# Optimization experiments

Measured on AMD Instinct MI355X. Metric: run time of the kernel, lower is better.

Reference implementation:

```python
import jax, jax.numpy as jnp
import numpy as np

L, D, H, F, K = 2, 256, 8, 512, 9
M, G1, G2, NT = 4, 40, 40, 2048
DH = D // H
KPD = 3  # per-dim neighbour window; KPD**2 == K


def setup_inputs() -> dict:
    key = jax.random.key(0)
    ks = jax.random.split(key, 16)
    s = 0.02
    ax0 = jnp.linspace(-1.0, 1.0, G1)
    ax1 = jnp.linspace(-1.0, 1.0, G2)
    gx, gy = jnp.meshgrid(ax0, ax1, indexing='ij')
    xc = jnp.broadcast_to(jnp.stack([gx, gy], -1), (M, G1, G2, 2))  # regular grid coords
    zc = jax.random.normal(ks[0], (M, G1, G2, D), dtype=jnp.float32)
    xt = jax.random.uniform(ks[1], (M, NT, 2), minval=-1.0, maxval=1.0)
    zt = jax.random.normal(ks[2], (M, NT, D), dtype=jnp.float32)
    def n(k, shape):
        return jax.random.normal(k, shape, dtype=jnp.float32) * s
    def ln():
        return jnp.stack([jnp.ones((L, D)), jnp.zeros((L, D))], 1)  # [L, 2(gamma,beta), D]
    return dict(
        xc=xc, zc=zc, xt=xt, zt=zt,
        sa_wqkv=n(ks[3], (L, D, 3 * D)), sa_wo=n(ks[4], (L, D, D)),
        sa_ln1=ln(), sa_ln2=ln(),
        sa_w1=n(ks[5], (L, D, F)), sa_b1=jnp.zeros((L, F)),
        sa_w2=n(ks[6], (L, F, D)), sa_b2=jnp.zeros((L, D)),
        ca_wq=n(ks[7], (L, D, D)), ca_wkv=n(ks[8], (L, D, 2 * D)), ca_wo=n(ks[9], (L, D, D)),
        ca_lnq=ln(), ca_lnkv=ln(), ca_ln2=ln(),
        ca_w1=n(ks[10], (L, D, F)), ca_b1=jnp.zeros((L, F)),
        ca_w2=n(ks[11], (L, F, D)), ca_b2=jnp.zeros((L, D)),
    )


def _ln(x, p):
    mu = x.mean(-1, keepdims=True)
    var = ((x - mu) ** 2).mean(-1, keepdims=True)
    return (x - mu) * jax.lax.rsqrt(var + 1e-5) * p[0] + p[1]


def nearest_gridded_neighbours(xt, xc):
    """Separable per-dim nearest grid index + KPD x KPD window, clamped at borders.
    Returns flat neighbour indices [M, NT, K] and validity mask [M, NT, K]."""
    ax0 = xc[:, :, 0, 0]  # [M, G1] axis-0 coordinates
    ax1 = xc[:, 0, :, 1]  # [M, G2] axis-1 coordinates
    n0 = jnp.argmin(jnp.abs(xt[..., 0:1] - ax0[:, None, :]), -1)  # [M, NT]
    n1 = jnp.argmin(jnp.abs(xt[..., 1:2] - ax1[:, None, :]), -1)
    off = jnp.arange(KPD) - KPD // 2
    r0 = n0[..., None] + off  # [M, NT, KPD]
    r1 = n1[..., None] + off
    v0 = (r0 >= 0) & (r0 < G1)
    v1 = (r1 >= 0) & (r1 < G2)
    i0 = jnp.clip(r0, 0, G1 - 1)
    i1 = jnp.clip(r1, 0, G2 - 1)
    idx = (i0[:, :, :, None] * G2 + i1[:, :, None, :]).reshape(xt.shape[0], -1, K)
    mask = (v0[:, :, :, None] & v1[:, :, None, :]).reshape(xt.shape[0], -1, K)
    return idx, mask


def reference(xc, zc, xt, zt, sa_wqkv, sa_wo, sa_ln1, sa_ln2, sa_w1, sa_b1, sa_w2, sa_b2,
              ca_wq, ca_wkv, ca_wo, ca_lnq, ca_lnkv, ca_ln2, ca_w1, ca_b1, ca_w2, ca_b2):
    m = zc.shape[0]
    idx, mask = nearest_gridded_neighbours(xt, xc)
    zc = zc.reshape(m, G1 * G2, D)  # flatten_grid
    bidx = jnp.arange(m)[:, None, None]
    scale = 1.0 / np.sqrt(DH)
    for l in range(L):
        # --- MHSA over flattened grid (pre-norm transformer block) ---
        h = _ln(zc, sa_ln1[l])
        q, k, v = jnp.split(h @ sa_wqkv[l], 3, -1)
        q = q.reshape(m, -1, H, DH); k = k.reshape(m, -1, H, DH); v = v.reshape(m, -1, H, DH)
        att = jax.nn.softmax(jnp.einsum('bnhd,bkhd->bhnk', q, k) * scale, -1)
        o = jnp.einsum('bhnk,bkhd->bnhd', att, v).reshape(m, -1, D)
        zc = zc + o @ sa_wo[l]
        h = _ln(zc, sa_ln2[l])
        zc = zc + jax.nn.gelu(h @ sa_w1[l] + sa_b1[l]) @ sa_w2[l] + sa_b2[l]
        # --- per-target masked MHCA over K nearest grid tokens (MATH SDPA path) ---
        nzc = zc[bidx, idx]  # [M, NT, K, D] neighbour gather
        q = (_ln(zt, ca_lnq[l]) @ ca_wq[l]).reshape(m, NT, H, DH)
        kk, vv = jnp.split(_ln(nzc, ca_lnkv[l]) @ ca_wkv[l], 2, -1)
        kk = kk.reshape(m, NT, K, H, DH); vv = vv.reshape(m, NT, K, H, DH)
        s = jnp.einsum('bnhd,bnkhd->bnhk', q, kk) * scale
        s = jnp.where(mask[:, :, None, :], s, -1e30)
        att = jax.nn.softmax(s, -1)
        o = jnp.einsum('bnhk,bnkhd->bnhd', att, vv).reshape(m, NT, D)
        zt = zt + o @ ca_wo[l]
        h = _ln(zt, ca_ln2[l])
        zt = zt + jax.nn.gelu(h @ ca_w1[l] + ca_b1[l]) @ ca_w2[l] + ca_b2[l]
    return zt
```

## Files before the change

### kernel.cpp

```cpp
#include <hip/hip_runtime.h>
#include <math.h>

#define LAYERS 2
#define DMODEL 256
#define NHEAD  8
#define DHEAD  32
#define FF     512
#define KNB    9
#define MB     4
#define G1D    40
#define G2D    40
#define NTGT   2048
#define NCTX   1600
#define RC     (MB*NCTX)
#define RT     (MB*NTGT)

typedef __attribute__((ext_vector_type(8))) short short8;
typedef __attribute__((ext_vector_type(4))) float f32x4;

#if __has_builtin(__builtin_amdgcn_exp2f)
#define EXP2(x) __builtin_amdgcn_exp2f(x)
#else
#define EXP2(x) exp2f(x)
#endif
#define L2E 1.4426950408889634f
#define ATTN_SCALE 0.17677669529663687f

#define ZC_OFF    0
#define HC_OFF    1638400
#define HT_OFF    (HC_OFF + 819200)
#define QKV_OFF   (HC_OFF + 2097152)
#define WT_OFF    (QKV_OFF + 3400000)
#define FB_OFF    (QKV_OFF + 4500000)
#define Q_OFF     (QKV_OFF + 4915200)
#define O_OFF     (Q_OFF + 2097152)
#define IDX_OFF   (O_OFF + 2097152)
#define MASK_OFF  (IDX_OFF + 73728)
#define WS_FLOATS (MASK_OFF + 73728)

#define WT_LAYER   1048576
#define WT_QKV     0
#define WT_WO      196608
#define WT_W1      262144
#define WT_W2      393216
#define WT_CWQ     524288
#define WT_CWKV    589824
#define WT_CWO     720896
#define WT_CW1     786432
#define WT_CW2     917504
#define FB_LAYER   2560
#define FB_QKV     0
#define FB_W1      768
#define FB_WKV     1280
#define FB_WQ      1792
#define FB_CW1     2048

static __device__ __forceinline__ float gelu_f(float x){
  float t = tanhf(0.7978845608028654f * (x + 0.044715f * x * x * x));
  return 0.5f * x * (1.0f + t);
}
static __device__ __forceinline__ unsigned int bf16_rne(float x){
  unsigned int u = __float_as_uint(x);
  return (u + 0x7fffu + ((u >> 16) & 1u)) >> 16;
}
static __device__ __forceinline__ unsigned int pack_bf16x2(float lo, float hi){
  return bf16_rne(lo) | (bf16_rne(hi) << 16);
}

struct TDesc { const float* src; const float* gamma; int dstoff; int K; int N; int nse; float nsc; };
struct TTable { TDesc e[18]; };

__global__ __launch_bounds__(256)
void wprep_kernel(TTable t, unsigned short* __restrict__ wt){
  TDesc d = t.e[blockIdx.z];
  int n0 = blockIdx.x * 32, k0 = blockIdx.y * 32;
  if (n0 >= d.N || k0 >= d.K) return;
  __shared__ float tile[32][33];
  int tx = threadIdx.x, ty = threadIdx.y;
  float csc = (n0 + tx < d.nse) ? d.nsc : 1.0f;
  #pragma unroll
  for (int j = 0; j < 4; j++){
    int k = k0 + ty * 4 + j;
    float v = d.src[(size_t)k * d.N + n0 + tx];
    if (d.gamma) v *= d.gamma[k];
    tile[ty * 4 + j][tx] = v * csc;
  }
  __syncthreads();
  #pragma unroll
  for (int j = 0; j < 4; j++)
    wt[(size_t)d.dstoff + (size_t)(n0 + ty * 4 + j) * d.K + k0 + tx] =
        (unsigned short)bf16_rne(tile[tx][ty * 4 + j]);
}

struct BDesc { const float* W; const float* beta; const float* base; int outoff; int N; int nse; float nsc; };
struct BTable { BDesc e[10]; };

__global__ __launch_bounds__(256)
void bfold_kernel(BTable t, float* __restrict__ fb){
  BDesc d = t.e[blockIdx.x];
  int n = blockIdx.y * 64 + (threadIdx.x >> 2);
  int q = threadIdx.x & 3;
  if (n >= d.N) return;
  float s = 0.f;
  #pragma unroll 4
  for (int k = q * 64; k < q * 64 + 64; k++)
    s += d.beta[k] * d.W[(size_t)k * d.N + n];
  s += __shfl_xor(s, 1);
  s += __shfl_xor(s, 2);
  if (q == 0){
    float r = s + (d.base ? d.base[n] : 0.f);
    if (n < d.nse) r *= d.nsc;
    fb[d.outoff + n] = r;
  }
}

__global__ void nn_idx_kernel(const float* __restrict__ xc, const float* __restrict__ xt,
                              int* __restrict__ idx, float* __restrict__ mask){
  int g = blockIdx.x * blockDim.x + threadIdx.x;
  if (g >= MB * NTGT) return;
  int m = g >> 11;
  float x0 = xt[(size_t)g * 2 + 0];
  float x1 = xt[(size_t)g * 2 + 1];
  const float* xcm = xc + (size_t)m * G1D * G2D * 2;
  int n0 = 0; float b0 = 1e30f;
  for (int i = 0; i < G1D; i++){
    float d = fabsf(x0 - xcm[i * (G2D * 2)]);
    if (d < b0){ b0 = d; n0 = i; }
  }
  int n1 = 0; float b1 = 1e30f;
  for (int j = 0; j < G2D; j++){
    float d = fabsf(x1 - xcm[j * 2 + 1]);
    if (d < b1){ b1 = d; n1 = j; }
  }
  #pragma unroll
  for (int a = 0; a < 3; a++){
    int r0 = n0 + a - 1;
    bool v0 = (r0 >= 0) && (r0 < G1D);
    int i0 = min(max(r0, 0), G1D - 1);
    #pragma unroll
    for (int b = 0; b < 3; b++){
      int r1 = n1 + b - 1;
      bool v1 = (r1 >= 0) && (r1 < G2D);
      int i1 = min(max(r1, 0), G2D - 1);
      idx [(size_t)g * KNB + a * 3 + b] = i0 * G2D + i1;
      mask[(size_t)g * KNB + a * 3 + b] = (v0 && v1) ? 1.0f : 0.0f;
    }
  }
}

__global__ __launch_bounds__(256)
void ln_norm(const float* __restrict__ x, unsigned short* __restrict__ y, int rows){
  int gw   = blockIdx.x * 4 + (threadIdx.x >> 6);
  int lane = threadIdx.x & 63;
  if (gw >= rows) return;
  const float* xr = x + (size_t)gw * DMODEL;
  int d0 = lane * 4;
  float4 xv = *(const float4*)(xr + d0);
  float s = xv.x + xv.y + xv.z + xv.w;
  #pragma unroll
  for (int off = 32; off > 0; off >>= 1) s += __shfl_xor(s, off);
  float mu = s * (1.0f / DMODEL);
  float dx0 = xv.x - mu, dx1 = xv.y - mu, dx2 = xv.z - mu, dx3 = xv.w - mu;
  float v = dx0*dx0 + dx1*dx1 + dx2*dx2 + dx3*dx3;
  #pragma unroll
  for (int off = 32; off > 0; off >>= 1) v += __shfl_xor(v, off);
  float rs = rsqrtf(v * (1.0f / DMODEL) + 1e-5f);
  uint2 w;
  w.x = pack_bf16x2(dx0 * rs, dx1 * rs);
  w.y = pack_bf16x2(dx2 * rs, dx3 * rs);
  *(uint2*)(y + (size_t)gw * DMODEL + d0) = w;
}

template<int ROWS>
static __device__ __forceinline__ void stage_glds(const unsigned short* __restrict__ src,
                                                  int Ksrc, unsigned short* lds,
                                                  int wave, int lane){
  #pragma unroll
  for (int j = 0; j < ROWS / 32; j++){
    int ublk = (j * 4 + wave) * 64;
    int u    = ublk + lane;
    int row  = u >> 3;
    int unit = (u & 7) ^ (row & 7);
    __builtin_amdgcn_global_load_lds(
        (const __attribute__((address_space(1))) void*)(src + (size_t)row * Ksrc + unit * 8),
        (__attribute__((address_space(3))) void*)(lds + (size_t)ublk * 8),
        16, 0, 0);
  }
}

template<int K, int MT, int NT>
__global__ __launch_bounds__(256)
void gemm_glds(const unsigned short* __restrict__ A, const unsigned short* __restrict__ Wt,
               const float* __restrict__ bias, const float* __restrict__ res,
               void* __restrict__ C, int N, int flags){
  const int MFR = MT / 32, NFR = NT / 32;
  __shared__ unsigned short Als[2][MT * 64];
  __shared__ unsigned short Bls[2][NT * 64];
  int tid = threadIdx.x;
  int wave = tid >> 6, lane = tid & 63;
  int wm = wave >> 1, wn = wave & 1;
  int l16 = lane & 15, grp = lane >> 4;
  int r0 = blockIdx.y * MT, c0 = blockIdx.x * NT;

  const unsigned short* Ag = A  + (size_t)r0 * K;
  const unsigned short* Bg = Wt + (size_t)c0 * K;
  const int nch = K >> 6;

  stage_glds<MT>(Ag, K, Als[0], wave, lane);
  stage_glds<NT>(Bg, K, Bls[0], wave, lane);

  f32x4 acc[MFR][NFR];
  #pragma unroll
  for (int m = 0; m < MFR; m++)
    #pragma unroll
    for (int n = 0; n < NFR; n++) acc[m][n] = (f32x4){0.f, 0.f, 0.f, 0.f};

  #pragma unroll
  for (int ch = 0; ch < nch; ch++){
    int b = ch & 1;
    __syncthreads();
    if (ch + 1 < nch){
      stage_glds<MT>(Ag + (ch + 1) * 64, K, Als[b ^ 1], wave, lane);
      stage_glds<NT>(Bg + (ch + 1) * 64, K, Bls[b ^ 1], wave, lane);
    }
    const unsigned short* Ab = Als[b];
    const unsigned short* Bb = Bls[b];
    #pragma unroll
    for (int kk = 0; kk < 2; kk++){
      short8 af[MFR], bfr[NFR];
      #pragma unroll
      for (int m = 0; m < MFR; m++){
        int row = wm * (MT / 2) + m * 16 + l16;
        int unit = (kk * 4 + grp) ^ (row & 7);
        af[m] = *(const short8*)(Ab + row * 64 + unit * 8);
      }
      #pragma unroll
      for (int n = 0; n < NFR; n++){
        int row = wn * (NT / 2) + n * 16 + l16;
        int unit = (kk * 4 + grp) ^ (row & 7);
        bfr[n] = *(const short8*)(Bb + row * 64 + unit * 8);
      }
      #pragma unroll
      for (int m = 0; m < MFR; m++)
        #pragma unroll
        for (int n = 0; n < NFR; n++)
          acc[m][n] = __builtin_amdgcn_mfma_f32_16x16x32_bf16(af[m], bfr[n], acc[m][n], 0, 0, 0);
    }
  }

  #pragma unroll
  for (int n = 0; n < NFR; n++){
    int gc = c0 + wn * (NT / 2) + n * 16 + l16;
    float bv = (flags & 1) ? bias[gc] : 0.f;
    #pragma unroll
    for (int m = 0; m < MFR; m++){
      int grb = r0 + wm * (MT / 2) + m * 16 + grp * 4;
      #pragma unroll
      for (int r = 0; r < 4; r++){
        float v = acc[m][n][r] + bv;
        if (flags & 2) v = gelu_f(v);
        if (flags & 4) v += res[(size_t)(grb + r) * N + gc];
        if (flags & 8) ((unsigned short*)C)[(size_t)(grb + r) * N + gc] = (unsigned short)bf16_rne(v);
        else           ((float*)C)[(size_t)(grb + r) * N + gc] = v;
      }
    }
  }
}

#define KSTR 42
#define VSTR 70
#define PSTR 70
__global__ __launch_bounds__(256)
void sa_attn_mfma(const unsigned short* __restrict__ qkv, unsigned short* __restrict__ ob){
  int m = blockIdx.z, h = blockIdx.y;
  int tid  = threadIdx.x;
  int wave = tid >> 6, lane = tid & 63;
  int qr = lane & 15, grp = lane >> 4;
  int q0 = blockIdx.x * 64 + wave * 16;

  __shared__ unsigned short Kls[2][64 * KSTR];
  __shared__ unsigned short Vls[2][32 * VSTR];
  __shared__ unsigned short Pls[4][16 * PSTR];
  unsigned short* Pw = Pls[wave];

  short8 qf = *(const short8*)(qkv + ((size_t)(m * NCTX + q0 + qr)) * 768 + h * 32 + grp * 8);

  int skey = tid >> 2;
  int scol = (tid & 3) * 8;
  const unsigned short* kbase = qkv + (size_t)m * NCTX * 768 + 256 + h * 32 + scol;

  uint4 kreg = *(const uint4*)(kbase + (size_t)skey * 768);
  uint4 vreg = *(const uint4*)(kbase + (size_t)skey * 768 + 256);

  float mq = -1e30f, lq = 0.0f;
  f32x4 acc0 = {0.f, 0.f, 0.f, 0.f};
  f32x4 acc1 = {0.f, 0.f, 0.f, 0.f};

  {
    *(uint4*)&Kls[0][skey * KSTR + scol] = kreg;
    unsigned int vv[4] = {vreg.x, vreg.y, vreg.z, vreg.w};
    #pragma unroll
    for (int j = 0; j < 4; j++){
      Vls[0][(scol + 2 * j    ) * VSTR + skey] = (unsigned short)(vv[j] & 0xffffu);
      Vls[0][(scol + 2 * j + 1) * VSTR + skey] = (unsigned short)(vv[j] >> 16);
    }
  }

  for (int kt = 0; kt < NCTX / 64; kt++){
    int b = kt & 1;
    __syncthreads();
    if (kt + 1 < NCTX / 64){
      kreg = *(const uint4*)(kbase + (size_t)((kt + 1) * 64 + skey) * 768);
      vreg = *(const uint4*)(kbase + (size_t)((kt + 1) * 64 + skey) * 768 + 256);
    }

    f32x4 s0 = {0.f,0.f,0.f,0.f}, s1 = {0.f,0.f,0.f,0.f};
    f32x4 s2 = {0.f,0.f,0.f,0.f}, s3 = {0.f,0.f,0.f,0.f};
    {
      const short8 k0 = *(const short8*)&Kls[b][( 0 + qr) * KSTR + grp * 8];
      const short8 k1 = *(const short8*)&Kls[b][(16 + qr) * KSTR + grp * 8];
      const short8 k2 = *(const short8*)&Kls[b][(32 + qr) * KSTR + grp * 8];
      const short8 k3 = *(const short8*)&Kls[b][(48 + qr) * KSTR + grp * 8];
      s0 = __builtin_amdgcn_mfma_f32_16x16x32_bf16(k0, qf, s0, 0, 0, 0);
      s1 = __builtin_amdgcn_mfma_f32_16x16x32_bf16(k1, qf, s1, 0, 0, 0);
      s2 = __builtin_amdgcn_mfma_f32_16x16x32_bf16(k2, qf, s2, 0, 0, 0);
      s3 = __builtin_amdgcn_mfma_f32_16x16x32_bf16(k3, qf, s3, 0, 0, 0);
    }

    float sc[4][4];
    #pragma unroll
    for (int r = 0; r < 4; r++){
      sc[0][r] = s0[r]; sc[1][r] = s1[r]; sc[2][r] = s2[r]; sc[3][r] = s3[r];
    }
    float tm = sc[0][0];
    #pragma unroll
    for (int kb = 0; kb < 4; kb++)
      #pragma unroll
      for (int r = 0; r < 4; r++) tm = fmaxf(tm, sc[kb][r]);
    tm = fmaxf(tm, __shfl_xor(tm, 16));
    tm = fmaxf(tm, __shfl_xor(tm, 32));
    float mn = fmaxf(mq, tm);
    float corr = EXP2(mq - mn);
    float ts = 0.f;
    float p[4][4];
    #pragma unroll
    for (int kb = 0; kb < 4; kb++)
      #pragma unroll
      for (int r = 0; r < 4; r++){
        float pv = EXP2(sc[kb][r] - mn);
        p[kb][r] = pv; ts += pv;
      }
    ts += __shfl_xor(ts, 16);
    ts += __shfl_xor(ts, 32);
    lq = lq * corr + ts;
    mq = mn;
    #pragma unroll
    for (int r = 0; r < 4; r++){ acc0[r] *= corr; acc1[r] *= corr; }

    #pragma unroll
    for (int kb = 0; kb < 4; kb++){
      *(unsigned int*)&Pw[qr * PSTR + kb * 16 + grp * 4]     = pack_bf16x2(p[kb][0], p[kb][1]);
      *(unsigned int*)&Pw[qr * PSTR + kb * 16 + grp * 4 + 2] = pack_bf16x2(p[kb][2], p[kb][3]);
    }

    #pragma unroll
    for (int hh = 0; hh < 2; hh++){
      const short8 pf = *(const short8*)&Pw[qr * PSTR + hh * 32 + grp * 8];
      const short8 v0 = *(const short8*)&Vls[b][( 0 + qr) * VSTR + hh * 32 + grp * 8];
      const short8 v1 = *(const short8*)&Vls[b][(16 + qr) * VSTR + hh * 32 + grp * 8];
      acc0 = __builtin_amdgcn_mfma_f32_16x16x32_bf16(v0, pf, acc0, 0, 0, 0);
      acc1 = __builtin_amdgcn_mfma_f32_16x16x32_bf16(v1, pf, acc1, 0, 0, 0);
    }

    if (kt + 1 < NCTX / 64){
      *(uint4*)&Kls[b ^ 1][skey * KSTR + scol] = kreg;
      unsigned int vv[4] = {vreg.x, vreg.y, vreg.z, vreg.w};
      #pragma unroll
      for (int j = 0; j < 4; j++){
        Vls[b ^ 1][(scol + 2 * j    ) * VSTR + skey] = (unsigned short)(vv[j] & 0xffffu);
        Vls[b ^ 1][(scol + 2 * j + 1) * VSTR + skey] = (unsigned short)(vv[j] >> 16);
      }
    }
  }

  float inv = 1.0f / lq;
  unsigned short* op = ob + ((size_t)(m * NCTX + q0 + qr)) * DMODEL + h * DHEAD;
  uint2 o16a, o16b;
  o16a.x = pack_bf16x2(acc0[0] * inv, acc0[1] * inv);
  o16a.y = pack_bf16x2(acc0[2] * inv, acc0[3] * inv);
  o16b.x = pack_bf16x2(acc1[0] * inv, acc1[1] * inv);
  o16b.y = pack_bf16x2(acc1[2] * inv, acc1[3] * inv);
  *(uint2*)(op + grp * 4)      = o16a;
  *(uint2*)(op + 16 + grp * 4) = o16b;
}

__global__ __launch_bounds__(256)
void ca_attn_kernel(const float* __restrict__ qb, const float* __restrict__ kv,
                    const int* __restrict__ idx, const float* __restrict__ mask,
                    unsigned short* __restrict__ ob){
  int g = blockIdx.x;
  int m = g >> 11;
  int tid = threadIdx.x;
  float q = qb[(size_t)g * DMODEL + tid];
  float s[KNB];
  int rws[KNB];
  #pragma unroll
  for (int k = 0; k < KNB; k++){
    int row = idx[(size_t)g * KNB + k];
    rws[k] = row;
    float p = q * kv[((size_t)(m * NCTX + row)) * 512 + tid];
    #pragma unroll
    for (int off = 16; off > 0; off >>= 1) p += __shfl_xor(p, off, 32);
    s[k] = (mask[(size_t)g * KNB + k] > 0.5f) ? p : -1e30f;
  }
  float sm = s[0];
  #pragma unroll
  for (int k = 1; k < KNB; k++) sm = fmaxf(sm, s[k]);
  float den = 0.f, w[KNB];
  #pragma unroll
  for (int k = 0; k < KNB; k++){ w[k] = __expf(s[k] - sm); den += w[k]; }
  float inv = 1.0f / den;
  float o = 0.f;
  #pragma unroll
  for (int k = 0; k < KNB; k++)
    o += w[k] * kv[((size_t)(m * NCTX + rws[k])) * 512 + 256 + tid];
  ob[(size_t)g * DMODEL + tid] = (unsigned short)bf16_rne(o * inv);
}

static inline void launch_gemm(const unsigned short* A, const unsigned short* Wt,
                               const float* bias, const float* res, void* C,
                               int R, int K, int N, int flags, hipStream_t stream){
  if (N == 768){
    gemm_glds<256, 64, 128><<<dim3(N / 128, R / 64), 256, 0, stream>>>(A, Wt, bias, res, C, N, flags);
  } else if (K == 256){
    gemm_glds<256, 64, 64><<<dim3(N / 64, R / 64), 256, 0, stream>>>(A, Wt, bias, res, C, N, flags);
  } else {
    gemm_glds<512, 64, 64><<<dim3(N / 64, R / 64), 256, 0, stream>>>(A, Wt, bias, res, C, N, flags);
  }
}

extern "C" void kernel_launch(void* const* d_in, const int* in_sizes, int n_in,
                              void* d_out, int out_size, void* d_ws, size_t ws_size,
                              hipStream_t stream){
  const float* xc      = (const float*)d_in[0];
  const float* zc_in   = (const float*)d_in[1];
  const float* xt      = (const float*)d_in[2];
  const float* zt_in   = (const float*)d_in[3];
  const float* sa_wqkv = (const float*)d_in[4];
  const float* sa_wo   = (const float*)d_in[5];
  const float* sa_ln1  = (const float*)d_in[6];
  const float* sa_ln2  = (const float*)d_in[7];
  const float* sa_w1   = (const float*)d_in[8];
  const float* sa_b1   = (const float*)d_in[9];
  const float* sa_w2   = (const float*)d_in[10];
  const float* sa_b2   = (const float*)d_in[11];
  const float* ca_wq   = (const float*)d_in[12];
  const float* ca_wkv  = (const float*)d_in[13];
  const float* ca_wo   = (const float*)d_in[14];
  const float* ca_lnq  = (const float*)d_in[15];
  const float* ca_lnkv = (const float*)d_in[16];
  const float* ca_ln2  = (const float*)d_in[17];
  const float* ca_w1   = (const float*)d_in[18];
  const float* ca_b1   = (const float*)d_in[19];
  const float* ca_w2   = (const float*)d_in[20];
  const float* ca_b2   = (const float*)d_in[21];

  if (ws_size < (size_t)WS_FLOATS * sizeof(float)) return;
  float* ws    = (float*)d_ws;
  float* zc    = ws + ZC_OFF;
  unsigned short* hc16 = (unsigned short*)(ws + HC_OFF);
  unsigned short* ht16 = (unsigned short*)(ws + HT_OFF);
  float* qkvb  = ws + QKV_OFF;
  unsigned short* qkv16 = (unsigned short*)qkvb;
  unsigned short* wt    = (unsigned short*)(ws + WT_OFF);
  float* fb    = ws + FB_OFF;
  float* qb    = ws + Q_OFF;
  unsigned short* ob16 = (unsigned short*)(ws + O_OFF);
  int*   idxb  = (int*)(ws + IDX_OFF);
  float* maskb = ws + MASK_OFF;
  float* zt    = (float*)d_out;

  const float QSC = ATTN_SCALE * L2E;

  TTable tt;
  for (int l = 0; l < LAYERS; l++){
    int b = l * WT_LAYER, i = l * 9;
    tt.e[i + 0] = { sa_wqkv + (size_t)l * 256 * 768, sa_ln1  + l * 512, b + WT_QKV,  256, 768, 256, QSC };
    tt.e[i + 1] = { sa_wo   + (size_t)l * 256 * 256, nullptr,           b + WT_WO,   256, 256, 0, 1.f };
    tt.e[i + 2] = { sa_w1   + (size_t)l * 256 * 512, sa_ln2  + l * 512, b + WT_W1,   256, 512, 0, 1.f };
    tt.e[i + 3] = { sa_w2   + (size_t)l * 512 * 256, nullptr,           b + WT_W2,   512, 256, 0, 1.f };
    tt.e[i + 4] = { ca_wq   + (size_t)l * 256 * 256, ca_lnq  + l * 512, b + WT_CWQ,  256, 256, 256, ATTN_SCALE };
    tt.e[i + 5] = { ca_wkv  + (size_t)l * 256 * 512, ca_lnkv + l * 512, b + WT_CWKV, 256, 512, 0, 1.f };
    tt.e[i + 6] = { ca_wo   + (size_t)l * 256 * 256, nullptr,           b + WT_CWO,  256, 256, 0, 1.f };
    tt.e[i + 7] = { ca_w1   + (size_t)l * 256 * 512, ca_ln2  + l * 512, b + WT_CW1,  256, 512, 0, 1.f };
    tt.e[i + 8] = { ca_w2   + (size_t)l * 512 * 256, nullptr,           b + WT_CW2,  512, 256, 0, 1.f };
  }
  wprep_kernel<<<dim3(24, 16, 18), dim3(32, 8), 0, stream>>>(tt, wt);

  BTable bt;
  for (int l = 0; l < LAYERS; l++){
    int fo = l * FB_LAYER, i = l * 5;
    bt.e[i + 0] = { sa_wqkv + (size_t)l * 256 * 768, sa_ln1  + l * 512 + 256, nullptr,        fo + FB_QKV, 768, 256, QSC };
    bt.e[i + 1] = { sa_w1   + (size_t)l * 256 * 512, sa_ln2  + l * 512 + 256, sa_b1 + l * FF, fo + FB_W1,  512, 0, 1.f };
    bt.e[i + 2] = { ca_wkv  + (size_t)l * 256 * 512, ca_lnkv + l * 512 + 256, nullptr,        fo + FB_WKV, 512, 0, 1.f };
    bt.e[i + 3] = { ca_wq   + (size_t)l * 256 * 256, ca_lnq  + l * 512 + 256, nullptr,        fo + FB_WQ,  256, 256, ATTN_SCALE };
    bt.e[i + 4] = { ca_w1   + (size_t)l * 256 * 512, ca_ln2  + l * 512 + 256, ca_b1 + l * FF, fo + FB_CW1, 512, 0, 1.f };
  }
  bfold_kernel<<<dim3(10, 12), 256, 0, stream>>>(bt, fb);

  nn_idx_kernel<<<(MB * NTGT) / 256, 256, 0, stream>>>(xc, xt, idxb, maskb);

  ln_norm<<<RC / 4, 256, 0, stream>>>(zc_in, hc16, RC);

  for (int l = 0; l < LAYERS; l++){
    const unsigned short* wl = wt + (size_t)l * WT_LAYER;
    const float* fl = fb + (size_t)l * FB_LAYER;
    const float* zc_src = (l == 0) ? zc_in : zc;
    const float* zt_src = (l == 0) ? zt_in : zt;

    launch_gemm(hc16, wl + WT_QKV, fl + FB_QKV, nullptr, qkv16, RC, 256, 768, 1 | 8, stream);
    sa_attn_mfma<<<dim3(NCTX / 64, NHEAD, MB), 256, 0, stream>>>(qkv16, ob16);
    launch_gemm(ob16, wl + WT_WO, nullptr, zc_src, zc, RC, 256, 256, 4, stream);
    ln_norm<<<RC / 4, 256, 0, stream>>>(zc, hc16, RC);
    launch_gemm(hc16, wl + WT_W1, fl + FB_W1, nullptr, qkv16, RC, 256, 512, 1 | 2 | 8, stream);
    launch_gemm(qkv16, wl + WT_W2, sa_b2 + l * DMODEL, zc, zc, RC, 512, 256, 1 | 4, stream);

    ln_norm<<<RC / 4, 256, 0, stream>>>(zc, hc16, RC);
    launch_gemm(hc16, wl + WT_CWKV, fl + FB_WKV, nullptr, qkvb, RC, 256, 512, 1, stream);
    ln_norm<<<RT / 4, 256, 0, stream>>>(zt_src, ht16, RT);
    launch_gemm(ht16, wl + WT_CWQ, fl + FB_WQ, nullptr, qb, RT, 256, 256, 1, stream);
    ca_attn_kernel<<<RT, 256, 0, stream>>>(qb, qkvb, idxb, maskb, ob16);
    launch_gemm(ob16, wl + WT_CWO, nullptr, zt_src, zt, RT, 256, 256, 4, stream);
    ln_norm<<<RT / 4, 256, 0, stream>>>(zt, ht16, RT);
    launch_gemm(ht16, wl + WT_CW1, fl + FB_CW1, nullptr, qkv16, RT, 256, 512, 1 | 2 | 8, stream);
    launch_gemm(qkv16, wl + WT_CW2, ca_b2 + l * DMODEL, zt, zt, RT, 512, 256, 1 | 4, stream);
  }
}
```

Measured before the change: 431.8 us.

## Split self-attention KV range into two halves with a merge kernel

Self-attention now splits the 25 key tiles into two ranges (13 and 12), launching twice as many blocks. Each block writes normalized partial outputs plus running max and sum, and a new merge kernel combines them with log-sum-exp weights. The goal is better GPU occupancy, since the original grid had only 800 blocks. The cost is an extra kernel launch, extra partial-buffer traffic, and an extra bf16 rounding of the partial outputs. LDS strides for K and P are also changed.

```diff
diff --git a/kernel.cpp b/kernel.cpp
--- a/kernel.cpp
+++ b/kernel.cpp
@@ -66,6 +66,9 @@
 static __device__ __forceinline__ unsigned int pack_bf16x2(float lo, float hi){
   return bf16_rne(lo) | (bf16_rne(hi) << 16);
 }
+static __device__ __forceinline__ float bfu(unsigned int u16){
+  return __uint_as_float(u16 << 16);
+}
 
 struct TDesc { const float* src; const float* gamma; int dstoff; int K; int N; int nse; float nsc; };
 struct TTable { TDesc e[18]; };
@@ -267,17 +270,23 @@
   }
 }
 
-#define KSTR 42
+#define KSTR 40
 #define VSTR 70
-#define PSTR 70
-__global__ __launch_bounds__(256)
-void sa_attn_mfma(const unsigned short* __restrict__ qkv, unsigned short* __restrict__ ob){
-  int m = blockIdx.z, h = blockIdx.y;
+#define PSTR 72
+__global__ __launch_bounds__(256)
+void sa_attn_mfma(const unsigned short* __restrict__ qkv,
+                  unsigned short* __restrict__ opart, float* __restrict__ mlb){
+  int mz = blockIdx.z;
+  int m = mz & 3, split = mz >> 2;
+  int h = blockIdx.y;
   int tid  = threadIdx.x;
   int wave = tid >> 6, lane = tid & 63;
   int qr = lane & 15, grp = lane >> 4;
   int q0 = blockIdx.x * 64 + wave * 16;
 
+  int kt0 = split * 13;
+  int kt1 = split ? (NCTX / 64) : 13;
+
   __shared__ unsigned short Kls[2][64 * KSTR];
   __shared__ unsigned short Vls[2][32 * VSTR];
   __shared__ unsigned short Pls[4][16 * PSTR];
@@ -289,8 +298,8 @@
   int scol = (tid & 3) * 8;
   const unsigned short* kbase = qkv + (size_t)m * NCTX * 768 + 256 + h * 32 + scol;
 
-  uint4 kreg = *(const uint4*)(kbase + (size_t)skey * 768);
-  uint4 vreg = *(const uint4*)(kbase + (size_t)skey * 768 + 256);
+  uint4 kreg = *(const uint4*)(kbase + (size_t)(kt0 * 64 + skey) * 768);
+  uint4 vreg = *(const uint4*)(kbase + (size_t)(kt0 * 64 + skey) * 768 + 256);
 
   float mq = -1e30f, lq = 0.0f;
   f32x4 acc0 = {0.f, 0.f, 0.f, 0.f};
@@ -306,10 +315,10 @@
     }
   }
 
-  for (int kt = 0; kt < NCTX / 64; kt++){
-    int b = kt & 1;
+  for (int kt = kt0; kt < kt1; kt++){
+    int b = (kt - kt0) & 1;
     __syncthreads();
-    if (kt + 1 < NCTX / 64){
+    if (kt + 1 < kt1){
       kreg = *(const uint4*)(kbase + (size_t)((kt + 1) * 64 + skey) * 768);
       vreg = *(const uint4*)(kbase + (size_t)((kt + 1) * 64 + skey) * 768 + 256);
     }
@@ -372,7 +381,7 @@
       acc1 = __builtin_amdgcn_mfma_f32_16x16x32_bf16(v1, pf, acc1, 0, 0, 0);
     }
 
-    if (kt + 1 < NCTX / 64){
+    if (kt + 1 < kt1){
       *(uint4*)&Kls[b ^ 1][skey * KSTR + scol] = kreg;
       unsigned int vv[4] = {vreg.x, vreg.y, vreg.z, vreg.w};
       #pragma unroll
@@ -384,7 +393,8 @@
   }
 
   float inv = 1.0f / lq;
-  unsigned short* op = ob + ((size_t)(m * NCTX + q0 + qr)) * DMODEL + h * DHEAD;
+  int gr = m * NCTX + q0 + qr;
+  unsigned short* op = opart + ((size_t)(split * RC + gr)) * DMODEL + h * DHEAD;
   uint2 o16a, o16b;
   o16a.x = pack_bf16x2(acc0[0] * inv, acc0[1] * inv);
   o16a.y = pack_bf16x2(acc0[2] * inv, acc0[3] * inv);
@@ -392,6 +402,39 @@
   o16b.y = pack_bf16x2(acc1[2] * inv, acc1[3] * inv);
   *(uint2*)(op + grp * 4)      = o16a;
   *(uint2*)(op + 16 + grp * 4) = o16b;
+  if (grp == 0){
+    float* mlp = mlb + ((size_t)(split * RC + gr)) * 16 + h * 2;
+    mlp[0] = mq;
+    mlp[1] = lq;
+  }
+}
+
+__global__ __launch_bounds__(256)
+void sa_merge(const unsigned short* __restrict__ opart, const float* __restrict__ mlb,
+              unsigned short* __restrict__ out){
+  int g = blockIdx.x * 256 + threadIdx.x;
+  int gr = g >> 6;
+  int d4 = (g & 63) * 4;
+  int h  = d4 >> 5;
+  float m1 = mlb[(size_t)gr * 16 + h * 2];
+  float l1 = mlb[(size_t)gr * 16 + h * 2 + 1];
+  float m2 = mlb[(size_t)(RC + gr) * 16 + h * 2];
+  float l2 = mlb[(size_t)(RC + gr) * 16 + h * 2 + 1];
+  float mm = fmaxf(m1, m2);
+  float w1 = l1 * EXP2(m1 - mm);
+  float w2 = l2 * EXP2(m2 - mm);
+  float inv = 1.0f / (w1 + w2);
+  w1 *= inv; w2 *= inv;
+  uint2 a = *(const uint2*)(opart + (size_t)gr * DMODEL + d4);
+  uint2 c = *(const uint2*)(opart + (size_t)(RC + gr) * DMODEL + d4);
+  float o0 = bfu(a.x & 0xffffu) * w1 + bfu(c.x & 0xffffu) * w2;
+  float o1 = bfu(a.x >> 16)     * w1 + bfu(c.x >> 16)     * w2;
+  float o2 = bfu(a.y & 0xffffu) * w1 + bfu(c.y & 0xffffu) * w2;
+  float o3 = bfu(a.y >> 16)     * w1 + bfu(c.y >> 16)     * w2;
+  uint2 w;
+  w.x = pack_bf16x2(o0, o1);
+  w.y = pack_bf16x2(o2, o3);
+  *(uint2*)(out + (size_t)gr * DMODEL + d4) = w;
 }
 
 __global__ __launch_bounds__(256)
@@ -475,7 +518,9 @@
   unsigned short* wt    = (unsigned short*)(ws + WT_OFF);
   float* fb    = ws + FB_OFF;
   float* qb    = ws + Q_OFF;
-  unsigned short* ob16 = (unsigned short*)(ws + O_OFF);
+  float* mlbuf = ws + Q_OFF;
+  unsigned short* ob16   = (unsigned short*)(ws + O_OFF);
+  unsigned short* opart16= (unsigned short*)(ws + O_OFF);
   int*   idxb  = (int*)(ws + IDX_OFF);
   float* maskb = ws + MASK_OFF;
   float* zt    = (float*)d_out;
@@ -519,8 +564,9 @@
     const float* zt_src = (l == 0) ? zt_in : zt;
 
     launch_gemm(hc16, wl + WT_QKV, fl + FB_QKV, nullptr, qkv16, RC, 256, 768, 1 | 8, stream);
-    sa_attn_mfma<<<dim3(NCTX / 64, NHEAD, MB), 256, 0, stream>>>(qkv16, ob16);
-    launch_gemm(ob16, wl + WT_WO, nullptr, zc_src, zc, RC, 256, 256, 4, stream);
+    sa_attn_mfma<<<dim3(NCTX / 64, NHEAD, MB * 2), 256, 0, stream>>>(qkv16, opart16, mlbuf);
+    sa_merge<<<RC * 64 / 256, 256, 0, stream>>>(opart16, mlbuf, ht16);
+    launch_gemm(ht16, wl + WT_WO, nullptr, zc_src, zc, RC, 256, 256, 4, stream);
     ln_norm<<<RC / 4, 256, 0, stream>>>(zc, hc16, RC);
     launch_gemm(hc16, wl + WT_W1, fl + FB_W1, nullptr, qkv16, RC, 256, 512, 1 | 2 | 8, stream);
     launch_gemm(qkv16, wl + WT_W2, sa_b2 + l * DMODEL, zc, zc, RC, 512, 256, 1 | 4, stream);
```

New measurement: 384.5 us. 1.12x faster.
